# Optimization experiments

Hardware: AMD Instinct MI355X
Metric: run time of the kernel (lower is better)

Reference implementation:

```python
import jax, jax.numpy as jnp
import numpy as np

B, N, M = 4, 512, 8192
QUERY_DIM, INPUT_DIM = 512, 256
HEADS, DIM_HEAD = 8, 64
ATT_DIM = HEADS * DIM_HEAD  # 512


def setup_inputs() -> dict:
    key = jax.random.key(0)
    ks = jax.random.split(key, 6)
    x = jax.random.normal(ks[0], (B, N, QUERY_DIM), dtype=jnp.float32)
    context = jax.random.normal(ks[1], (B, M, INPUT_DIM), dtype=jnp.float32)
    # Linear weights stored as [in, out] for x @ W
    Wq = jax.random.normal(ks[2], (QUERY_DIM, ATT_DIM), dtype=jnp.float32) / np.sqrt(QUERY_DIM)
    Wkv = jax.random.normal(ks[3], (INPUT_DIM, 2 * ATT_DIM), dtype=jnp.float32) / np.sqrt(INPUT_DIM)
    Wo = jax.random.normal(ks[4], (ATT_DIM, QUERY_DIM), dtype=jnp.float32) / np.sqrt(ATT_DIM)
    bo = jax.random.normal(ks[5], (QUERY_DIM,), dtype=jnp.float32) * 0.01
    return {"x": x, "context": context, "Wq": Wq, "Wkv": Wkv, "Wo": Wo, "bo": bo}


def reference(x, context, Wq, Wkv, Wo, bo):
    scale = DIM_HEAD ** -0.5
    q = x @ Wq                      # [B, N, H*D]
    kv = context @ Wkv              # [B, M, 2*H*D]
    k, v = jnp.split(kv, 2, axis=-1)
    # split heads: b n (h d) -> b h n d
    q = q.reshape(B, N, HEADS, DIM_HEAD).transpose(0, 2, 1, 3)
    k = k.reshape(B, M, HEADS, DIM_HEAD).transpose(0, 2, 1, 3)
    v = v.reshape(B, M, HEADS, DIM_HEAD).transpose(0, 2, 1, 3)
    scores = jnp.einsum('bhid,bhjd->bhij', q, k) * scale  # [B, H, N, M]
    attn = jax.nn.softmax(scores, axis=-1)
    out = jnp.einsum('bhij,bhjd->bhid', attn, v)           # [B, H, N, D]
    out = out.transpose(0, 2, 1, 3).reshape(B, N, ATT_DIM)
    return out @ Wo + bo
```

## Files before the change

kernel.cpp:

```cpp
#include <hip/hip_runtime.h>
#include <hip/hip_bf16.h>
#include <cstdint>

#define NB 4
#define NQ 512
#define NM 8192
#define NH 8
#define DH 64

typedef short bf16x8s __attribute__((ext_vector_type(8)));
typedef short bf16x4s __attribute__((ext_vector_type(4)));
typedef float f32x4  __attribute__((ext_vector_type(4)));

static __device__ __forceinline__ short f2bs(float f) {
    unsigned u = __builtin_bit_cast(unsigned, f);
    return (short)(unsigned short)((u + 0x8000u) >> 16);
}
static __device__ __forceinline__ unsigned pk2(float a, float b) {
    unsigned au = __builtin_bit_cast(unsigned, a) + 0x8000u;
    unsigned bu = __builtin_bit_cast(unsigned, b) + 0x8000u;
    return __builtin_amdgcn_perm(bu, au, 0x07060302u);
}

#if __has_builtin(__builtin_amdgcn_exp2f)
static __device__ __forceinline__ float fexp2(float x) { return __builtin_amdgcn_exp2f(x); }
#else
static __device__ __forceinline__ float fexp2(float x) { return exp2f(x); }
#endif

__global__ __launch_bounds__(256) void prep_weights(
    const float* __restrict__ Wq, const float* __restrict__ Wo,
    const float* __restrict__ Wkv,
    short* __restrict__ Wqf, short* __restrict__ Wof, short* __restrict__ Wkvf)
{
    const int t = threadIdx.x;
    const int w = t >> 6, ln = t & 63;
    const int m16 = ln & 15, quad = ln >> 4;
    int f = blockIdx.x * 4 + w;
    const float* src; short* dst; int N, KS, n0, ks;
    if (f < 512)       { src = Wq;  dst = Wqf;  N = 512;  KS = 16; n0 = f >> 4; ks = f & 15; }
    else if (f < 1024) { f -= 512;  src = Wo;  dst = Wof;  N = 512;  KS = 16; n0 = f >> 4; ks = f & 15; }
    else               { f -= 1024; src = Wkv; dst = Wkvf; N = 1024; KS = 8;  n0 = f >> 3; ks = f & 7; }
    const float* sp = src + (size_t)(ks * 32 + quad * 8) * N + n0 * 16 + m16;
    float v[8];
    #pragma unroll
    for (int j = 0; j < 8; ++j) v[j] = sp[(size_t)j * N];
    uint4 pkv = { pk2(v[0],v[1]), pk2(v[2],v[3]), pk2(v[4],v[5]), pk2(v[6],v[7]) };
    *(uint4*)(dst + ((size_t)(n0 * KS + ks) * 64 + ln) * 8) = pkv;
}

__device__ __forceinline__ void proj32_body(
    const float* __restrict__ A, const short* __restrict__ Wf,
    float* __restrict__ C, const float* __restrict__ bias,
    int tm, int tn, char* smemraw, int t)
{
    short* As = (short*)smemraw;

    const int w = t >> 6, ln = t & 63;
    const int m16 = ln & 15, quad = ln >> 4;
    const int wm = w >> 1, wn = w & 1;

    const int ar = t >> 3, ac = (t & 7) << 3;

    const float* Ap = A + (size_t)(tm * 32 + ar) * 512 + ac;

    f32x4 acc[2] = {};

    {
        float4 a0 = *(const float4*)(Ap);
        float4 a1 = *(const float4*)(Ap + 4);
        uint4 wa = { pk2(a0.x,a0.y), pk2(a0.z,a0.w), pk2(a1.x,a1.y), pk2(a1.z,a1.w) };
        *(uint4*)&As[ar * 72 + ac] = wa;
    }

    #pragma unroll
    for (int k0 = 0; k0 < 512; k0 += 64) {
        short* Ab = As + ((k0 >> 6) & 1) * 2304;
        __syncthreads();

        bf16x8s bfr[2][2];
        #pragma unroll
        for (int ks = 0; ks < 2; ++ks)
            #pragma unroll
            for (int nt = 0; nt < 2; ++nt)
                bfr[ks][nt] = *(const bf16x8s*)(Wf +
                    ((size_t)((tn * 4 + wn * 2 + nt) * 16 + (k0 >> 5) + ks) * 64 + ln) * 8);

        bf16x8s afr[2];
        #pragma unroll
        for (int ks = 0; ks < 2; ++ks)
            afr[ks] = *(const bf16x8s*)&Ab[(wm * 16 + m16) * 72 + ks * 32 + quad * 8];

        float4 a0n, a1n;
        if (k0 + 64 < 512) {
            a0n = *(const float4*)(Ap + k0 + 64);
            a1n = *(const float4*)(Ap + k0 + 68);
        }

        #pragma unroll
        for (int ks = 0; ks < 2; ++ks)
            #pragma unroll
            for (int nt = 0; nt < 2; ++nt)
                acc[nt] = __builtin_amdgcn_mfma_f32_16x16x32_bf16(afr[ks], bfr[ks][nt], acc[nt], 0, 0, 0);

        if (k0 + 64 < 512) {
            short* Abn = As + ((((k0 >> 6) + 1) & 1)) * 2304;
            uint4 wa = { pk2(a0n.x,a0n.y), pk2(a0n.z,a0n.w), pk2(a1n.x,a1n.y), pk2(a1n.z,a1n.w) };
            *(uint4*)&Abn[ar * 72 + ac] = wa;
        }
    }

    const int row0 = tm * 32 + wm * 16 + quad * 4;
    const int col0 = tn * 64 + wn * 32;
    #pragma unroll
    for (int nt = 0; nt < 2; ++nt) {
        const int col = col0 + nt * 16 + m16;
        const float bb = bias ? bias[col] : 0.f;
        #pragma unroll
        for (int r = 0; r < 4; ++r)
            C[(size_t)(row0 + r) * 512 + col] = acc[nt][r] + bb;
    }
}

__device__ __forceinline__ void kv_body(
    const float* __restrict__ A, const short* __restrict__ Wkvf,
    short* __restrict__ Kf, short* __restrict__ Vf,
    int kvid, char* smemraw)
{
    short* As = (short*)smemraw;

    const int t  = threadIdx.x;
    const int tm  = ((kvid >> 6) << 3) | (kvid & 7);
    const int tn0 = (kvid >> 3) & 7;
    const int w  = t >> 6, ln = t & 63;
    const int m16 = ln & 15, quad = ln >> 4;
    const int wm = w & 1, wn = w >> 1;

    const int ar = t >> 2;
    const int ac = (t & 3) << 3;

    const float* Abase = A + (size_t)(tm * 128 + ar) * 256 + ac;

    f32x4 acc[4][2] = {};

    for (int s = 0; s < 8; ++s) {
        float4 a0 = *(const float4*)(Abase + s * 32);
        float4 a1 = *(const float4*)(Abase + s * 32 + 4);
        __syncthreads();
        uint4 wa = { pk2(a0.x,a0.y), pk2(a0.z,a0.w), pk2(a1.x,a1.y), pk2(a1.z,a1.w) };
        *(uint4*)&As[ar * 40 + ac] = wa;
        __syncthreads();

        bf16x8s bfr[2];
        #pragma unroll
        for (int j = 0; j < 2; ++j)
            bfr[j] = *(const bf16x8s*)(Wkvf +
                ((size_t)((tn0 * 8 + wn * 2 + j) * 8 + s) * 64 + ln) * 8);

        #pragma unroll
        for (int i = 0; i < 4; ++i) {
            bf16x8s af = *(const bf16x8s*)&As[(wm * 64 + i * 16 + m16) * 40 + quad * 8];
            acc[i][0] = __builtin_amdgcn_mfma_f32_16x16x32_bf16(af, bfr[0], acc[i][0], 0, 0, 0);
            acc[i][1] = __builtin_amdgcn_mfma_f32_16x16x32_bf16(af, bfr[1], acc[i][1], 0, 0, 0);
        }
    }

    const int row0 = tm * 128;
    const int b    = row0 >> 13;
    const int mr0  = row0 & (NM - 1);
    const int g0   = mr0 >> 5;

    __syncthreads();
    short* S = (short*)smemraw + w * 1024;

    if (tn0 < 4) {
        const int h = tn0 * 2 + (wn >> 1);
        short* Kp = Kf + (size_t)(b * NH + h) * (NM * DH);
        const int ksel = wn & 1;
        #pragma unroll
        for (int hf = 0; hf < 2; ++hf) {
            #pragma unroll
            for (int di = 0; di < 2; ++di) {
                const int i = hf * 2 + di;
                #pragma unroll
                for (int j = 0; j < 2; ++j) {
                    const int base = (quad & 1) * 512 + (j * 2 + (m16 >> 3)) * 128
                                   + ((di * 2 + (quad >> 1)) * 4) * 8 + (m16 & 7);
                    #pragma unroll
                    for (int r = 0; r < 4; ++r)
                        S[base + r * 8] = f2bs(acc[i][j][r]);
                }
            }
            const int g = g0 + wm * 2 + hf;
            #pragma unroll
            for (int fl = 0; fl < 2; ++fl) {
                uint4 v = *(const uint4*)&S[fl * 512 + ln * 8];
                *(uint4*)(Kp + ((size_t)((g * 2 + fl) * 2 + ksel) * 512 + ln * 8)) = v;
            }
        }
    } else {
        const int h = (tn0 - 4) * 2 + (wn >> 1);
        short* Vp = Vf + (size_t)(b * NH + h) * (NM * DH);
        #pragma unroll
        for (int hf = 0; hf < 2; ++hf) {
            #pragma unroll
            for (int di = 0; di < 2; ++di) {
                const int i = hf * 2 + di;
                #pragma unroll
                for (int j = 0; j < 2; ++j) {
                    const int base = j * 512
                                   + ((di * 2 + (quad >> 1)) * 16 + m16) * 8
                                   + (quad & 1) * 4;
                    #pragma unroll
                    for (int r = 0; r < 4; ++r)
                        S[base + r] = f2bs(acc[i][j][r]);
                }
            }
            const int g = g0 + wm * 2 + hf;
            #pragma unroll
            for (int fl = 0; fl < 2; ++fl) {
                uint4 v = *(const uint4*)&S[fl * 512 + ln * 8];
                *(uint4*)(Vp + ((size_t)((((wn & 1) * 2 + fl) * 256 + g) * 64 + ln) * 8)) = v;
            }
        }
    }
}

__global__ __launch_bounds__(512, 4) void gemm_kvq(
    const float* __restrict__ x,   const short* __restrict__ Wqf, float* __restrict__ q,
    const float* __restrict__ ctx, const short* __restrict__ Wkvf,
    short* __restrict__ Kf, short* __restrict__ Vf)
{
    __shared__ __align__(16) char smem[18432];
    if (blockIdx.x < 256) {
        const int u = (int)(blockIdx.x * 2) + (int)(threadIdx.x >> 8);
        proj32_body(x, Wqf, q, nullptr, u >> 3, u & 7,
                    smem + (threadIdx.x >> 8) * 9216, (int)(threadIdx.x & 255));
    } else {
        kv_body(ctx, Wkvf, Kf, Vf, (int)(blockIdx.x - 256), smem);
    }
}

__global__ __launch_bounds__(256) void gemm_proj32(
    const float* __restrict__ A, const short* __restrict__ Wf,
    float* __restrict__ C, const float* __restrict__ bias)
{
    __shared__ __align__(16) char smem[32 * 72 * 2 * 2];
    proj32_body(A, Wf, C, bias, (int)(blockIdx.x >> 3), (int)(blockIdx.x & 7),
                smem, (int)threadIdx.x);
}

__global__ __launch_bounds__(512, 4) void attn_mfma(
    const float* __restrict__ Q,
    const short* __restrict__ Kfr,
    const short* __restrict__ Vfr,
    float* __restrict__ Og)
{
    __shared__ __align__(16) float Ob[2][32 * 66];
    __shared__ float lbuf[8 * 32];

    const int bid = blockIdx.x;
    const int xcd = bid & 7, g = bid >> 3;
    const int bh  = xcd * 4 + (g & 3);
    const int qt  = g >> 2;
    const int b   = bh >> 3, h = bh & 7;
    const int t   = threadIdx.x;
    const int w   = t >> 6, ln = t & 63;
    const int m16 = ln & 15, quad = ln >> 4;

    const short* Kbase = Kfr + (size_t)bh * (NM * DH);
    const short* Vbase = Vfr + (size_t)bh * (NM * DH);

    const float qsc = 0.125f * 1.44269504f;
    bf16x8s qf[2][2];
    #pragma unroll
    for (int mt = 0; mt < 2; ++mt) {
        const float* qrow = Q + ((size_t)(b * NQ + qt * 32 + mt * 16 + m16)) * 512 + h * 64;
        #pragma unroll
        for (int ks = 0; ks < 2; ++ks) {
            float4 x0 = *(const float4*)(qrow + ks * 32 + quad * 8);
            float4 x1 = *(const float4*)(qrow + ks * 32 + quad * 8 + 4);
            uint4 pkv = { pk2(x0.x * qsc, x0.y * qsc), pk2(x0.z * qsc, x0.w * qsc),
                          pk2(x1.x * qsc, x1.y * qsc), pk2(x1.z * qsc, x1.w * qsc) };
            qf[mt][ks] = *reinterpret_cast<bf16x8s*>(&pkv);
        }
    }

    bf16x8s ones8;
    #pragma unroll
    for (int j = 0; j < 8; ++j) ones8[j] = (short)0x3F80;

    f32x4 o[2][4] = {};
    f32x4 lsum[2] = {};

    bf16x8s kf[4][2];
    {
        const int kc = w * 64;
        #pragma unroll
        for (int nt = 0; nt < 4; ++nt)
            #pragma unroll
            for (int ks = 0; ks < 2; ++ks)
                kf[nt][ks] = *(const bf16x8s*)(Kbase + ((((kc >> 4) + nt) * 2 + ks) << 9) + ln * 8);
    }

    for (int it = 0; it < 16; ++it) {
        const int kc = it * 512 + w * 64;

        bf16x8s va8[4][2];
        #pragma unroll
        for (int dt = 0; dt < 4; ++dt)
            #pragma unroll
            for (int gg = 0; gg < 2; ++gg)
                va8[dt][gg] = *(const bf16x8s*)(Vbase + ((size_t)(dt * 256 + (kc >> 5) + gg) * 64 + ln) * 8);

        f32x4 st[2][4] = {};
        #pragma unroll
        for (int kt = 0; kt < 4; ++kt)
            #pragma unroll
            for (int mt = 0; mt < 2; ++mt) {
                st[mt][kt] = __builtin_amdgcn_mfma_f32_16x16x32_bf16(kf[kt][0], qf[mt][0], st[mt][kt], 0, 0, 0);
                st[mt][kt] = __builtin_amdgcn_mfma_f32_16x16x32_bf16(kf[kt][1], qf[mt][1], st[mt][kt], 0, 0, 0);
            }

        if (it + 1 < 16) {
            const int kn = (it + 1) * 512 + w * 64;
            #pragma unroll
            for (int nt = 0; nt < 4; ++nt)
                #pragma unroll
                for (int ks = 0; ks < 2; ++ks)
                    kf[nt][ks] = *(const bf16x8s*)(Kbase + ((((kn >> 4) + nt) * 2 + ks) << 9) + ln * 8);
        }

        #pragma unroll
        for (int mt = 0; mt < 2; ++mt)
            #pragma unroll
            for (int gg = 0; gg < 2; ++gg) {
                const f32x4 s0 = st[mt][2 * gg];
                const f32x4 s1 = st[mt][2 * gg + 1];
                uint4 pu = { pk2(fexp2(s0[0]), fexp2(s0[1])), pk2(fexp2(s0[2]), fexp2(s0[3])),
                             pk2(fexp2(s1[0]), fexp2(s1[1])), pk2(fexp2(s1[2]), fexp2(s1[3])) };
                bf16x8s pbv = *reinterpret_cast<bf16x8s*>(&pu);
                #pragma unroll
                for (int dt = 0; dt < 4; ++dt)
                    o[mt][dt] = __builtin_amdgcn_mfma_f32_16x16x32_bf16(va8[dt][gg], pbv, o[mt][dt], 0, 0, 0);
                lsum[mt] = __builtin_amdgcn_mfma_f32_16x16x32_bf16(ones8, pbv, lsum[mt], 0, 0, 0);
            }
    }

    if (quad == 0) {
        #pragma unroll
        for (int mt = 0; mt < 2; ++mt)
            lbuf[w * 32 + mt * 16 + m16] = lsum[mt][0];
    }
    if (w < 2) {
        float* dst = Ob[w];
        #pragma unroll
        for (int mt = 0; mt < 2; ++mt)
            #pragma unroll
            for (int dt = 0; dt < 4; ++dt)
                *(f32x4*)&dst[(mt * 16 + m16) * 66 + dt * 16 + quad * 4] = o[mt][dt];
    }
    __syncthreads();
    #pragma unroll
    for (int ph = 1; ph < 4; ++ph) {
        if ((w >> 1) == ph) {
            float* dst = Ob[w & 1];
            #pragma unroll
            for (int mt = 0; mt < 2; ++mt)
                #pragma unroll
                for (int dt = 0; dt < 4; ++dt) {
                    float* p = &dst[(mt * 16 + m16) * 66 + dt * 16 + quad * 4];
                    f32x4 cur = *(f32x4*)p;
                    cur += o[mt][dt];
                    *(f32x4*)p = cur;
                }
        }
        __syncthreads();
    }
    {
        const int row = t >> 4;
        const int d0  = (t & 15) << 2;
        float l = 0.f;
        #pragma unroll
        for (int wi = 0; wi < 8; ++wi) l += lbuf[wi * 32 + row];
        const float inv = 1.0f / l;
        float* op = Og + ((size_t)(b * NQ + qt * 32 + row)) * 512 + h * 64 + d0;
        const int c = row * 66 + d0;
        float4 r;
        r.x = (Ob[0][c + 0] + Ob[1][c + 0]) * inv;
        r.y = (Ob[0][c + 1] + Ob[1][c + 1]) * inv;
        r.z = (Ob[0][c + 2] + Ob[1][c + 2]) * inv;
        r.w = (Ob[0][c + 3] + Ob[1][c + 3]) * inv;
        *(float4*)op = r;
    }
}

extern "C" void kernel_launch(void* const* d_in, const int* in_sizes, int n_in,
                              void* d_out, int out_size, void* d_ws, size_t ws_size,
                              hipStream_t stream) {
    (void)in_sizes; (void)n_in; (void)out_size; (void)ws_size;

    const float* x   = (const float*)d_in[0];
    const float* ctx = (const float*)d_in[1];
    const float* Wq  = (const float*)d_in[2];
    const float* Wkv = (const float*)d_in[3];
    const float* Wo  = (const float*)d_in[4];
    const float* bo  = (const float*)d_in[5];
    float* out = (float*)d_out;

    float* ws    = (float*)d_ws;
    float* q     = ws;
    float* attno = q + (size_t)2048 * 512;
    short* Kf    = (short*)(attno + (size_t)2048 * 512);
    short* Vf    = Kf + (size_t)NB * NH * NM * DH;
    short* Wqf   = Vf + (size_t)NB * NH * NM * DH;
    short* Wof   = Wqf + (size_t)512 * 512;
    short* Wkvf  = Wof + (size_t)512 * 512;

    prep_weights<<<dim3(384), dim3(256), 0, stream>>>(Wq, Wo, Wkv, Wqf, Wof, Wkvf);

    gemm_kvq<<<dim3(2304), dim3(512), 0, stream>>>(x, Wqf, q, ctx, Wkvf, Kf, Vf);

    attn_mfma<<<dim3(512), dim3(512), 0, stream>>>(q, Kf, Vf, attno);

    gemm_proj32<<<dim3(512), dim3(256), 0, stream>>>(attno, Wof, out, bo);
}
```

Baseline: 172.4 us.

## Emit attention output as bf16 and add an LDS-free bf16 output projection

The attention kernel now writes its normalized output as packed bf16 rather than fp32. The output projection is replaced by a new kernel that loads those bf16 A fragments directly from global memory into MFMA operands, with no LDS staging or fp32-to-bf16 conversion. s_setprio is also raised around the MFMA blocks in the attention loop so those waves get issue priority. The intent is to halve the intermediate traffic and simplify the final GEMM. The cost is an extra bf16 rounding step on the attention output, which was already rounded before the MFMA previously.

New measurement: 445.7 us. +158.6%, slower.

```diff
diff --git a/kernel.cpp b/kernel.cpp
--- a/kernel.cpp
+++ b/kernel.cpp
@@ -241,20 +241,59 @@
     }
 }
 
-__global__ __launch_bounds__(256) void gemm_proj32(
-    const float* __restrict__ A, const short* __restrict__ Wf,
+__global__ __launch_bounds__(256) void gemm_projb(
+    const short* __restrict__ Ab, const short* __restrict__ Wf,
     float* __restrict__ C, const float* __restrict__ bias)
 {
-    __shared__ __align__(16) char smem[32 * 72 * 2 * 2];
-    proj32_body(A, Wf, C, bias, (int)(blockIdx.x >> 3), (int)(blockIdx.x & 7),
-                smem, (int)threadIdx.x);
+    const int tm = (int)(blockIdx.x >> 3), tn = (int)(blockIdx.x & 7);
+    const int t = (int)threadIdx.x;
+    const int w = t >> 6, ln = t & 63;
+    const int m16 = ln & 15, quad = ln >> 4;
+    const int wm = w >> 1, wn = w & 1;
+
+    const short* Ap = Ab + (size_t)(tm * 32 + wm * 16 + m16) * 512 + quad * 8;
+
+    f32x4 acc[2] = {};
+
+    #pragma unroll
+    for (int k0 = 0; k0 < 512; k0 += 64) {
+        bf16x8s bfr[2][2];
+        #pragma unroll
+        for (int ks = 0; ks < 2; ++ks)
+            #pragma unroll
+            for (int nt = 0; nt < 2; ++nt)
+                bfr[ks][nt] = *(const bf16x8s*)(Wf +
+                    ((size_t)((tn * 4 + wn * 2 + nt) * 16 + (k0 >> 5) + ks) * 64 + ln) * 8);
+
+        bf16x8s afr[2];
+        #pragma unroll
+        for (int ks = 0; ks < 2; ++ks)
+            afr[ks] = *(const bf16x8s*)(Ap + k0 + ks * 32);
+
+        #pragma unroll
+        for (int ks = 0; ks < 2; ++ks)
+            #pragma unroll
+            for (int nt = 0; nt < 2; ++nt)
+                acc[nt] = __builtin_amdgcn_mfma_f32_16x16x32_bf16(afr[ks], bfr[ks][nt], acc[nt], 0, 0, 0);
+    }
+
+    const int row0 = tm * 32 + wm * 16 + quad * 4;
+    const int col0 = tn * 64 + wn * 32;
+    #pragma unroll
+    for (int nt = 0; nt < 2; ++nt) {
+        const int col = col0 + nt * 16 + m16;
+        const float bb = bias[col];
+        #pragma unroll
+        for (int r = 0; r < 4; ++r)
+            C[(size_t)(row0 + r) * 512 + col] = acc[nt][r] + bb;
+    }
 }
 
 __global__ __launch_bounds__(512, 4) void attn_mfma(
     const float* __restrict__ Q,
     const short* __restrict__ Kfr,
     const short* __restrict__ Vfr,
-    float* __restrict__ Og)
+    short* __restrict__ Ogb)
 {
     __shared__ __align__(16) float Ob[2][32 * 66];
     __shared__ float lbuf[8 * 32];
@@ -314,6 +353,7 @@
                 va8[dt][gg] = *(const bf16x8s*)(Vbase + ((size_t)(dt * 256 + (kc >> 5) + gg) * 64 + ln) * 8);
 
         f32x4 st[2][4] = {};
+        __builtin_amdgcn_s_setprio(1);
         #pragma unroll
         for (int kt = 0; kt < 4; ++kt)
             #pragma unroll
@@ -321,6 +361,7 @@
                 st[mt][kt] = __builtin_amdgcn_mfma_f32_16x16x32_bf16(kf[kt][0], qf[mt][0], st[mt][kt], 0, 0, 0);
                 st[mt][kt] = __builtin_amdgcn_mfma_f32_16x16x32_bf16(kf[kt][1], qf[mt][1], st[mt][kt], 0, 0, 0);
             }
+        __builtin_amdgcn_s_setprio(0);
 
         if (it + 1 < 16) {
             const int kn = (it + 1) * 512 + w * 64;
@@ -340,10 +381,12 @@
                 uint4 pu = { pk2(fexp2(s0[0]), fexp2(s0[1])), pk2(fexp2(s0[2]), fexp2(s0[3])),
                              pk2(fexp2(s1[0]), fexp2(s1[1])), pk2(fexp2(s1[2]), fexp2(s1[3])) };
                 bf16x8s pbv = *reinterpret_cast<bf16x8s*>(&pu);
+                __builtin_amdgcn_s_setprio(1);
                 #pragma unroll
                 for (int dt = 0; dt < 4; ++dt)
                     o[mt][dt] = __builtin_amdgcn_mfma_f32_16x16x32_bf16(va8[dt][gg], pbv, o[mt][dt], 0, 0, 0);
                 lsum[mt] = __builtin_amdgcn_mfma_f32_16x16x32_bf16(ones8, pbv, lsum[mt], 0, 0, 0);
+                __builtin_amdgcn_s_setprio(0);
             }
     }
 
@@ -384,14 +427,14 @@
         #pragma unroll
         for (int wi = 0; wi < 8; ++wi) l += lbuf[wi * 32 + row];
         const float inv = 1.0f / l;
-        float* op = Og + ((size_t)(b * NQ + qt * 32 + row)) * 512 + h * 64 + d0;
         const int c = row * 66 + d0;
-        float4 r;
-        r.x = (Ob[0][c + 0] + Ob[1][c + 0]) * inv;
-        r.y = (Ob[0][c + 1] + Ob[1][c + 1]) * inv;
-        r.z = (Ob[0][c + 2] + Ob[1][c + 2]) * inv;
-        r.w = (Ob[0][c + 3] + Ob[1][c + 3]) * inv;
-        *(float4*)op = r;
+        const float v0 = (Ob[0][c + 0] + Ob[1][c + 0]) * inv;
+        const float v1 = (Ob[0][c + 1] + Ob[1][c + 1]) * inv;
+        const float v2 = (Ob[0][c + 2] + Ob[1][c + 2]) * inv;
+        const float v3 = (Ob[0][c + 3] + Ob[1][c + 3]) * inv;
+        uint2 rv = { pk2(v0, v1), pk2(v2, v3) };
+        short* op = Ogb + ((size_t)(b * NQ + qt * 32 + row)) * 512 + h * 64 + d0;
+        *(uint2*)op = rv;
     }
 }
 
@@ -410,8 +453,8 @@
 
     float* ws    = (float*)d_ws;
     float* q     = ws;
-    float* attno = q + (size_t)2048 * 512;
-    short* Kf    = (short*)(attno + (size_t)2048 * 512);
+    short* attnb = (short*)(q + (size_t)2048 * 512);
+    short* Kf    = attnb + (size_t)2048 * 512;
     short* Vf    = Kf + (size_t)NB * NH * NM * DH;
     short* Wqf   = Vf + (size_t)NB * NH * NM * DH;
     short* Wof   = Wqf + (size_t)512 * 512;
@@ -421,7 +464,7 @@
 
     gemm_kvq<<<dim3(2304), dim3(512), 0, stream>>>(x, Wqf, q, ctx, Wkvf, Kf, Vf);
 
-    attn_mfma<<<dim3(512), dim3(512), 0, stream>>>(q, Kf, Vf, attno);
-
-    gemm_proj32<<<dim3(512), dim3(256), 0, stream>>>(attno, Wof, out, bo);
-}
+    attn_mfma<<<dim3(512), dim3(512), 0, stream>>>(q, Kf, Vf, attnb);
+
+    gemm_projb<<<dim3(512), dim3(256), 0, stream>>>(attnb, Wof, out, bo);
+}
```
